# Kernel optimization log

Hardware: AMD Instinct MI355X
Metric: run time of the kernel (lower is better)

## Reference

```python
import jax, jax.numpy as jnp
import numpy as np
import math

N, H, E, G = 20000, 256, 320000, 1000
NF, NS = 64, 3           # sinusoid frequencies, spatial dims
DIS = 2 * NF * NS        # 384
EIN = 2 * H + 9 + DIS    # edge MLP input dim = 905


def silu(x):
    return x * jax.nn.sigmoid(x)


def sin_emb(x):
    # x: [E, 3] -> [E, 2*NF*3]
    freqs = 2.0 * math.pi * jnp.arange(NF, dtype=x.dtype)
    emb = (x[..., None] * freqs).reshape(x.shape[0], NF * NS)
    return jnp.concatenate([jnp.sin(emb), jnp.cos(emb)], axis=-1)


def layer_norm(x, gamma, beta, eps=1e-5):
    mu = jnp.mean(x, axis=-1, keepdims=True)
    var = jnp.var(x, axis=-1, keepdims=True)
    return (x - mu) * jax.lax.rsqrt(var + eps) * gamma + beta


def setup_inputs() -> dict:
    key = jax.random.key(0)
    ks = jax.random.split(key, 16)
    s = 0.02
    return {
        "node_features": jax.random.normal(ks[0], (N, H), jnp.float32),
        "lattices": jax.random.normal(ks[1], (G, 3, 3), jnp.float32),
        "edge_index": jax.random.randint(ks[2], (2, E), 0, N, dtype=jnp.int64),
        "edge2graph": jnp.sort(jax.random.randint(ks[3], (E,), 0, G, dtype=jnp.int64)),
        "frac_diff": jax.random.uniform(ks[4], (E, NS), jnp.float32),
        "num_atoms": jax.random.randint(ks[5], (G,), 0, 100, dtype=jnp.int64),
        "ln_gamma": jnp.ones((H,), jnp.float32),
        "ln_beta": jnp.zeros((H,), jnp.float32),
        "We1": jax.random.normal(ks[6], (EIN, H), jnp.float32) * s,
        "be1": jnp.zeros((H,), jnp.float32),
        "We2": jax.random.normal(ks[7], (H, H), jnp.float32) * s,
        "be2": jnp.zeros((H,), jnp.float32),
        "Wn1": jax.random.normal(ks[8], (2 * H, H), jnp.float32) * s,
        "bn1": jnp.zeros((H,), jnp.float32),
        "Wn2": jax.random.normal(ks[9], (H, H), jnp.float32) * s,
        "bn2": jnp.zeros((H,), jnp.float32),
    }


def reference(node_features, lattices, edge_index, edge2graph, frac_diff, num_atoms,
              ln_gamma, ln_beta, We1, be1, We2, be2, Wn1, bn1, Wn2, bn2):
    n = node_features.shape[0]
    h = layer_norm(node_features, ln_gamma, ln_beta)

    # edge model: gather + concat + MLP
    hi = h[edge_index[0]]                      # [E, H]
    hj = h[edge_index[1]]                      # [E, H]
    fd = sin_emb(frac_diff)                    # [E, DIS]
    ltl = jnp.einsum('gij,gkj->gik', lattices, lattices).reshape(-1, 9)  # non_symmetric: L @ L^T
    le = ltl[edge2graph]                       # [E, 9]
    x = jnp.concatenate([hi, hj, le, fd], axis=1)        # [E, EIN]
    e = silu(x @ We1 + be1)
    e = silu(e @ We2 + be2)                    # [E, H]

    # node model: scatter-mean + concat + MLP
    src = edge_index[0]
    sums = jax.ops.segment_sum(e, src, num_segments=n)   # [N, H]
    cnt = jax.ops.segment_sum(jnp.ones((e.shape[0],), e.dtype), src, num_segments=n)
    agg = sums / jnp.maximum(cnt, 1.0)[:, None]
    y = jnp.concatenate([h, agg], axis=1)                # [N, 2H]
    y = silu(y @ Wn1 + bn1)
    y = silu(y @ Wn2 + bn2)

    return node_features + y
```

## Files before the change

### kernel.cpp

```cpp
#include <hip/hip_runtime.h>

typedef unsigned short UST;
typedef __bf16 bf16x8 __attribute__((ext_vector_type(8)));
typedef float floatx4 __attribute__((ext_vector_type(4)));
typedef unsigned short ushort8v __attribute__((ext_vector_type(8)));
typedef unsigned short ushort4v __attribute__((ext_vector_type(4)));

#define N_NODES 20000
#define E_EDGES 320000
#define KF 384
#define M_PAD 20096


static __device__ __forceinline__ UST f2bf(float x){
  unsigned int u = __float_as_uint(x);
  u += 0x7fffu + ((u >> 16) & 1u);
  return (UST)(u >> 16);
}
static __device__ __forceinline__ float bf2f(UST u){
  return __uint_as_float(((unsigned int)u) << 16);
}
static __device__ __forceinline__ float siluf(float v){
  return v * __builtin_amdgcn_rcpf(1.0f + __expf(-v));
}
static __device__ __forceinline__ unsigned int cvtpk(float lo, float hi){
  unsigned int r;
  asm("v_cvt_pk_bf16_f32 %0, %1, %2" : "=v"(r) : "v"(lo), "v"(hi));
  return r;
}
static __device__ __forceinline__ void gll16(const void* g, void* lds){
  __builtin_amdgcn_global_load_lds(
      (const __attribute__((address_space(1))) unsigned int*)g,
      (__attribute__((address_space(3))) unsigned int*)lds, 16, 0, 0);
}

static __device__ __forceinline__ void mfma_step(const UST* As, const UST* Bs,
    floatx4 (&acc)[4][4], int lm, int quad, int wM, int wN){
  bf16x8 a[4], b[4];
#pragma unroll
  for (int i = 0; i < 4; ++i)
    a[i] = *(const bf16x8*)(As + (wM + i*16 + lm)*32 + quad*8);
#pragma unroll
  for (int i = 0; i < 4; ++i)
    b[i] = *(const bf16x8*)(Bs + (wN + i*16 + lm)*32 + quad*8);
#pragma unroll
  for (int mi = 0; mi < 4; ++mi)
#pragma unroll
    for (int ni = 0; ni < 4; ++ni)
      acc[mi][ni] = __builtin_amdgcn_mfma_f32_16x16x32_bf16(a[mi], b[ni], acc[mi][ni], 0, 0, 0);
}

static __device__ __forceinline__ void mfma_stage2(const UST* At, const UST* Bg,
    int Kb, floatx4 (&acc)[4][4], int lm, int quad, int wM, int wN){
#pragma unroll 2
  for (int k0 = 0; k0 < 256; k0 += 32){
    bf16x8 a[4], b[4];
#pragma unroll
    for (int i = 0; i < 4; ++i)
      a[i] = *(const bf16x8*)(At + (wM + i*16 + lm)*264 + k0 + quad*8);
#pragma unroll
    for (int i = 0; i < 4; ++i)
      b[i] = *(const bf16x8*)(Bg + (size_t)(wN + i*16 + lm)*Kb + k0 + quad*8);
#pragma unroll
    for (int mi = 0; mi < 4; ++mi)
#pragma unroll
      for (int ni = 0; ni < 4; ++ni)
        acc[mi][ni] = __builtin_amdgcn_mfma_f32_16x16x32_bf16(a[mi], b[ni], acc[mi][ni], 0, 0, 0);
  }
}

__global__ __launch_bounds__(256) void prep_all(
    const float* __restrict__ We1, const float* __restrict__ We2,
    const float* __restrict__ Wn1, const float* __restrict__ Wn2,
    const float* __restrict__ x, const float* __restrict__ gamma,
    const float* __restrict__ beta, const float* __restrict__ lat,
    const int* __restrict__ esrc, const float* __restrict__ be1,
    int* __restrict__ cnti,
    UST* __restrict__ W1T, UST* __restrict__ W2T,
    UST* __restrict__ Wn1T, UST* __restrict__ Wn2T, UST* __restrict__ W1hT,
    UST* __restrict__ h, float* __restrict__ Pleb){
  int bid = blockIdx.x, t = threadIdx.x;
  if (bid < 384){
    int i = bid*256 + t;
    int n = i / KF, k = i % KF;
    W1T[i] = f2bf(We1[(size_t)(521 + (k&1)*192 + (k>>1))*256 + n]);
  } else if (bid < 640){
    int i = (bid-384)*256 + t;
    int n = i >> 8, k = i & 255;
    W2T[i]  = f2bf(We2[(size_t)k*256 + n]);
    Wn2T[i] = f2bf(Wn2[(size_t)k*256 + n]);
  } else if (bid < 1152){
    int i = (bid-640)*256 + t;
    int n = i >> 9, k = i & 511;
    Wn1T[i] = f2bf(Wn1[(size_t)k*256 + n]);
  } else if (bid < 1664){
    int n = bid - 1152, k = t;
    W1hT[n*256 + k] = f2bf(We1[(size_t)(k + (n & 256))*256 + (n & 255)]);
  } else if (bid < 6664){
    int wave = t >> 6, lane = t & 63;
    int row = (bid-1664)*4 + wave;
    const float4* xp = (const float4*)(x + (size_t)row * 256);
    float4 v = xp[lane];
    float s  = v.x + v.y + v.z + v.w;
    float sq = v.x*v.x + v.y*v.y + v.z*v.z + v.w*v.w;
#pragma unroll
    for (int o = 32; o > 0; o >>= 1){ s += __shfl_xor(s, o); sq += __shfl_xor(sq, o); }
    float mu  = s * (1.0f/256.0f);
    float var = sq * (1.0f/256.0f) - mu*mu;
    float rs  = rsqrtf(var + 1e-5f);
    float4 g = ((const float4*)gamma)[lane];
    float4 b = ((const float4*)beta)[lane];
    uint2 o2;
    o2.x = cvtpk((v.x-mu)*rs*g.x + b.x, (v.y-mu)*rs*g.y + b.y);
    o2.y = cvtpk((v.z-mu)*rs*g.z + b.z, (v.w-mu)*rs*g.w + b.w);
    *(uint2*)(h + (size_t)row*256 + lane*4) = o2;
  } else if (bid < 7664){
    int g = bid - 6664;
    const float* L = lat + g*9;
    float acc = be1[t];
#pragma unroll
    for (int a = 0; a < 3; ++a)
#pragma unroll
      for (int b = 0; b < 3; ++b){
        float ltlv = L[a*3+0]*L[b*3+0] + L[a*3+1]*L[b*3+1] + L[a*3+2]*L[b*3+2];
        acc += ltlv * We1[(size_t)(512 + a*3 + b)*256 + t];
      }
    int tp = (t & 0xC0) | ((t & 15) << 2) | ((t >> 4) & 3);
    Pleb[g*256 + tp] = acc;
  } else {
    int e = (bid-7664)*256 + t;
    if (e < E_EDGES) atomicAdd(&cnti[esrc[e]], 1);
  }
}

__global__ __launch_bounds__(256) void scan_kernel(const int* __restrict__ cnti,
    int* __restrict__ off, int* __restrict__ head){
  __shared__ int ps[256];
  int t = threadIdx.x;
  const int CH = 80;
  const int4* cp = (const int4*)cnti;
  int base = t * CH;
  int s = 0;
#pragma unroll 1
  for (int i = 0; i < CH/4; ++i){
    int4 v = cp[t*(CH/4) + i];
    int idx = base + i*4;
    if (idx   < N_NODES) s += v.x;
    if (idx+1 < N_NODES) s += v.y;
    if (idx+2 < N_NODES) s += v.z;
    if (idx+3 < N_NODES) s += v.w;
  }
  ps[t] = s; __syncthreads();
#pragma unroll 1
  for (int o = 1; o < 256; o <<= 1){
    int v = (t >= o) ? ps[t - o] : 0;
    __syncthreads();
    ps[t] += v;
    __syncthreads();
  }
  int run = (t > 0) ? ps[t-1] : 0;
#pragma unroll 1
  for (int i = 0; i < CH/4; ++i){
    int4 v = cp[t*(CH/4) + i];
    int idx = base + i*4;
    int a4[4] = {v.x, v.y, v.z, v.w};
#pragma unroll
    for (int j = 0; j < 4; ++j){
      int id = idx + j;
      if (id < N_NODES){ off[id] = run; head[id] = run; run += a4[j]; }
    }
  }
  if (t == 255) off[N_NODES] = run;
}

__global__ __launch_bounds__(256) void fill_kernel(const int* __restrict__ src,
    int* __restrict__ head, int* __restrict__ eidx, int* __restrict__ srcs){
  int e = blockIdx.x*256 + threadIdx.x;
  if (e < E_EDGES){
    int s = src[e];
    int p = atomicAdd(&head[s], 1);
    eidx[p] = e;
    srcs[p] = s;
  }
}

__global__ __launch_bounds__(256, 4)
void gemm_p1(const UST* __restrict__ h, const UST* __restrict__ B1,
             float* __restrict__ P1){
  __shared__ __attribute__((aligned(16))) UST lds[20480];
  UST* As0 = lds;
  UST* As1 = lds + 2048;
  UST* Bs0 = lds + 4096;
  UST* Bs1 = lds + 12288;
  int t = threadIdx.x;
  int bM = blockIdx.x >> 1, bN = (blockIdx.x & 1) << 8;
  int rA = t >> 2, cA = (t & 3) * 8;
  const UST* hrow = h + (size_t)(bM*64 + rA)*256;
  int lane = t & 63, lm = lane & 15, quad = lane >> 4;
  int wave = t >> 6, wN = wave*64;
  floatx4 acc[4][4] = {};
  UST* a0d = &As0[rA*32 + cA];
  UST* a1d = &As1[rA*32 + cA];
#pragma unroll 1
  for (int w = 0; w < 4; ++w){
    int k0 = w*64;
    gll16(hrow + k0 + cA,      a0d);
    gll16(hrow + k0 + 32 + cA, a1d);
#pragma unroll
    for (int j = 0; j < 4; ++j){
      int rB = j*64 + rA;
      gll16(B1 + (size_t)(bN + rB)*256 + k0 + cA,      &Bs0[rB*32 + cA]);
      gll16(B1 + (size_t)(bN + rB)*256 + k0 + 32 + cA, &Bs1[rB*32 + cA]);
    }
    __syncthreads();
    mfma_step(As0, Bs0, acc, lm, quad, 0, wN);
    mfma_step(As1, Bs1, acc, lm, quad, 0, wN);
    __syncthreads();
  }
  int mbase = bM*64 + quad*4;
#pragma unroll
  for (int mi = 0; mi < 4; ++mi)
#pragma unroll
    for (int r = 0; r < 4; ++r){
      int m = mbase + mi*16 + r;
      float4 v;
      v.x = acc[mi][0][r]; v.y = acc[mi][1][r];
      v.z = acc[mi][2][r]; v.w = acc[mi][3][r];
      *(float4*)(P1 + (size_t)m*512 + bN + wN + lm*4) = v;
    }
}

__global__ __launch_bounds__(512, 4)
void gemm_edge_fused(const int* __restrict__ ei, const int* __restrict__ e2g,
                     const float* __restrict__ fdif, const UST* __restrict__ W1T,
                     const int* __restrict__ eidx,
                     const UST* __restrict__ W2T, const float* __restrict__ be2,
                     const int* __restrict__ rownode,
                     const float* __restrict__ P1, const float* __restrict__ Pleb,
                     float* __restrict__ sums){
  __shared__ __attribute__((aligned(16))) UST lds[128*264];
  __shared__ int rn[128], rd[128], rg[128];
  UST* Ab0 = lds;
  UST* Ab1 = lds + 4096;
  UST* Bb0 = lds + 8192;
  UST* Bb1 = lds + 16384;
  UST* e1t = lds;
  UST* EsT = lds;
  int t = threadIdx.x;
  int bM = blockIdx.x;
  int rA = t >> 2, cA = (t & 3) * 8;
  int p0 = bM*128 + rA;
  int e0 = eidx[p0];
  float f0x = fdif[e0*3+0], f0y = fdif[e0*3+1], f0z = fdif[e0*3+2];
  size_t btb0 = (size_t)rA*KF + cA;
  size_t btb1 = btb0 + (size_t)128*KF;
  int lane = t & 63, lm = lane & 15, quad = lane >> 4;
  int wave = t >> 6, wM = (wave >> 2)*64, wN = (wave & 3)*64;
  floatx4 acc[4][4] = {};
  if (t < 128){
    int e = eidx[bM*128 + t];
    rn[t] = rownode[bM*128 + t];
    rd[t] = ei[E_EDGES + e];
    rg[t] = e2g[e];
  }

  float sdx = __builtin_amdgcn_sinf(f0x), cdx = __builtin_amdgcn_cosf(f0x);
  float sdy = __builtin_amdgcn_sinf(f0y), cdy = __builtin_amdgcn_cosf(f0y);
  float sdz = __builtin_amdgcn_sinf(f0z), cdz = __builtin_amdgcn_cosf(f0z);

  auto buildA = [&](int s)->uint4 {
    int j0 = s*16 + (cA >> 1);
    int dim = j0 >> 6;
    float fr = (dim == 0) ? f0x : ((dim == 1) ? f0y : f0z);
    float sd = (dim == 0) ? sdx : ((dim == 1) ? sdy : sdz);
    float cd = (dim == 0) ? cdx : ((dim == 1) ? cdy : cdz);
    float q  = __builtin_amdgcn_fractf(fr * (float)(j0 & 63));
    float sn = __builtin_amdgcn_sinf(q);
    float cs = __builtin_amdgcn_cosf(q);
    uint4 o;
    o.x = cvtpk(sn, cs);
    float s2;
    s2 = fmaf(sn, cd, cs*sd); cs = fmaf(cs, cd, -sn*sd); sn = s2; o.y = cvtpk(sn, cs);
    s2 = fmaf(sn, cd, cs*sd); cs = fmaf(cs, cd, -sn*sd); sn = s2; o.z = cvtpk(sn, cs);
    s2 = fmaf(sn, cd, cs*sd); cs = fmaf(cs, cd, -sn*sd); sn = s2; o.w = cvtpk(sn, cs);
    return o;
  };

  {
    uint4 o = buildA(0);
    *(uint4*)&Ab0[rA*32 + cA] = o;
    gll16(W1T + btb0, &Bb0[rA*32 + cA]);
    gll16(W1T + btb1, &Bb0[(128+rA)*32 + cA]);
  }
  __syncthreads();
#pragma unroll 1
  for (int s = 0; s < 12; ++s){
    UST* Ac = (s & 1) ? Ab1 : Ab0;
    UST* Bc = (s & 1) ? Bb1 : Bb0;
    if (s < 11){
      uint4 o = buildA(s+1);
      UST* An = (s & 1) ? Ab0 : Ab1;
      UST* Bn = (s & 1) ? Bb0 : Bb1;
      *(uint4*)&An[rA*32 + cA] = o;
      int k0 = (s+1)*32;
      gll16(W1T + btb0 + k0, &Bn[rA*32 + cA]);
      gll16(W1T + btb1 + k0, &Bn[(128+rA)*32 + cA]);
    }
    mfma_step(Ac, Bc, acc, lm, quad, wM, wN);
    __syncthreads();
  }

#pragma unroll
  for (int mi = 0; mi < 4; ++mi){
    int ml0 = wM + mi*16 + quad*4;
    float bs[4][4];
#pragma unroll
    for (int r = 0; r < 4; ++r){
      int ml = ml0 + r;
      float4 a4 = *(const float4*)(P1   + (size_t)rn[ml]*512 + wN + lm*4);
      float4 b4 = *(const float4*)(P1   + (size_t)rd[ml]*512 + 256 + wN + lm*4);
      float4 c4 = *(const float4*)(Pleb + (size_t)rg[ml]*256 + wN + lm*4);
      bs[r][0] = a4.x + b4.x + c4.x;
      bs[r][1] = a4.y + b4.y + c4.y;
      bs[r][2] = a4.z + b4.z + c4.z;
      bs[r][3] = a4.w + b4.w + c4.w;
    }
#pragma unroll
    for (int ni = 0; ni < 4; ++ni){
      int nl = wN + ni*16 + lm;
      float f0 = siluf(acc[mi][ni][0] + bs[0][ni]);
      float f1 = siluf(acc[mi][ni][1] + bs[1][ni]);
      float f2 = siluf(acc[mi][ni][2] + bs[2][ni]);
      float f3 = siluf(acc[mi][ni][3] + bs[3][ni]);
      unsigned w01 = cvtpk(f0, f1);
      unsigned w23 = cvtpk(f2, f3);
      e1t[(ml0+0)*264 + nl] = (UST)(w01 & 0xffffu);
      e1t[(ml0+1)*264 + nl] = (UST)(w01 >> 16);
      e1t[(ml0+2)*264 + nl] = (UST)(w23 & 0xffffu);
      e1t[(ml0+3)*264 + nl] = (UST)(w23 >> 16);
    }
  }
  __syncthreads();

  floatx4 acc2[4][4] = {};
  mfma_stage2(e1t, W2T, 256, acc2, lm, quad, wM, wN);
  __syncthreads();

#pragma unroll
  for (int mi = 0; mi < 4; ++mi)
#pragma unroll
    for (int ni = 0; ni < 4; ++ni){
      int nl = wN + ni*16 + lm;
      int ml = wM + mi*16 + quad*4;
      float b = be2[nl];
      uint2 pk2;
      pk2.x = cvtpk(siluf(acc2[mi][ni][0] + b), siluf(acc2[mi][ni][1] + b));
      pk2.y = cvtpk(siluf(acc2[mi][ni][2] + b), siluf(acc2[mi][ni][3] + b));
      *(uint2*)&EsT[nl*132 + ml] = pk2;
    }
  __syncthreads();
  {
    int c = t & 255, hh = t >> 8;
    int rbeg = hh * 64;
    int cur = rn[rbeg];
    float run = 0.0f;
#pragma unroll 1
    for (int r = rbeg; r < rbeg + 64; r += 4){
      ushort4v v4 = *(const ushort4v*)&EsT[c*132 + r];
#pragma unroll
      for (int q2 = 0; q2 < 4; ++q2){
        int nd = rn[r + q2];
        if (nd != cur){ atomicAdd(&sums[(size_t)cur*256 + c], run); run = 0.0f; cur = nd; }
        run += bf2f(v4[q2]);
      }
    }
    atomicAdd(&sums[(size_t)cur*256 + c], run);
  }
}

__global__ __launch_bounds__(256, 4)
void gemm_node12(const UST* __restrict__ h, const float* __restrict__ sums,
                 const int* __restrict__ offs, const UST* __restrict__ B1,
                 const float* __restrict__ bn1, const UST* __restrict__ B2,
                 const float* __restrict__ bn2,
                 float* __restrict__ out_f, const float* __restrict__ resid){
  __shared__ __attribute__((aligned(16))) UST lds[20480];
  UST* As0 = lds;
  UST* As1 = lds + 2048;
  UST* Bs0 = lds + 4096;
  UST* Bs1 = lds + 12288;
  UST* y1t = lds;
  int t = threadIdx.x;
  int bM = blockIdx.x;
  int rA = t >> 2, cA = (t & 3) * 8;
  int row = bM*64 + rA;
  bool valid = row < N_NODES;
  float inv = 0.0f;
  if (valid){
    int deg = offs[row+1] - offs[row];
    inv = 1.0f / fmaxf((float)deg, 1.0f);
  }
  const UST* hrow = h + (size_t)row*256;
  const float* srow = sums + (size_t)row*256;
  int lane = t & 63, lm = lane & 15, quad = lane >> 4;
  int wave = t >> 6, wN = wave*64;
  floatx4 acc[4][4] = {};
  UST* a0d = &As0[rA*32 + cA];
  UST* a1d = &As1[rA*32 + cA];
  const uint4 z4 = {0,0,0,0};
#pragma unroll 1
  for (int w = 0; w < 8; ++w){
    int k0 = w*64;
    if (k0 < 256){
      if (valid){
        gll16(hrow + k0 + cA,      a0d);
        gll16(hrow + k0 + 32 + cA, a1d);
      } else {
        *(uint4*)a0d = z4;
        *(uint4*)a1d = z4;
      }
    } else {
      uint4 o0 = z4, o1 = z4;
      if (valid){
        int q = k0 - 256 + cA;
        float4 s0 = *(const float4*)(srow + q);
        float4 s1 = *(const float4*)(srow + q + 4);
        o0.x = cvtpk(s0.x*inv, s0.y*inv); o0.y = cvtpk(s0.z*inv, s0.w*inv);
        o0.z = cvtpk(s1.x*inv, s1.y*inv); o0.w = cvtpk(s1.z*inv, s1.w*inv);
        float4 s2 = *(const float4*)(srow + q + 32);
        float4 s3 = *(const float4*)(srow + q + 36);
        o1.x = cvtpk(s2.x*inv, s2.y*inv); o1.y = cvtpk(s2.z*inv, s2.w*inv);
        o1.z = cvtpk(s3.x*inv, s3.y*inv); o1.w = cvtpk(s3.z*inv, s3.w*inv);
      }
      *(uint4*)a0d = o0;
      *(uint4*)a1d = o1;
    }
#pragma unroll
    for (int j = 0; j < 4; ++j){
      int rB = j*64 + rA;
      gll16(B1 + (size_t)rB*512 + k0 + cA,      &Bs0[rB*32 + cA]);
      gll16(B1 + (size_t)rB*512 + k0 + 32 + cA, &Bs1[rB*32 + cA]);
    }
    __syncthreads();
    mfma_step(As0, Bs0, acc, lm, quad, 0, wN);
    mfma_step(As1, Bs1, acc, lm, quad, 0, wN);
    __syncthreads();
  }
#pragma unroll
  for (int mi = 0; mi < 4; ++mi){
    int ml0 = mi*16 + quad*4;
#pragma unroll
    for (int ni = 0; ni < 4; ++ni){
      int nl = wN + ni*16 + lm;
      float b = bn1[nl];
      unsigned w01 = cvtpk(siluf(acc[mi][ni][0] + b), siluf(acc[mi][ni][1] + b));
      unsigned w23 = cvtpk(siluf(acc[mi][ni][2] + b), siluf(acc[mi][ni][3] + b));
      y1t[(ml0+0)*264 + nl] = (UST)(w01 & 0xffffu);
      y1t[(ml0+1)*264 + nl] = (UST)(w01 >> 16);
      y1t[(ml0+2)*264 + nl] = (UST)(w23 & 0xffffu);
      y1t[(ml0+3)*264 + nl] = (UST)(w23 >> 16);
    }
  }
  __syncthreads();
  floatx4 acc2[4][4] = {};
  mfma_stage2(y1t, B2, 256, acc2, lm, quad, 0, wN);
  int mbase = bM*64 + quad*4;
  int nbase = wN + lm;
#pragma unroll
  for (int mi = 0; mi < 4; ++mi)
#pragma unroll
    for (int r = 0; r < 4; ++r){
      int m = mbase + mi*16 + r;
      if (m < N_NODES){
#pragma unroll
        for (int ni = 0; ni < 4; ++ni){
          int n = nbase + ni*16;
          float v = siluf(acc2[mi][ni][r] + bn2[n]);
          out_f[(size_t)m*256 + n] = resid[(size_t)m*256 + n] + v;
        }
      }
    }
}

extern "C" void kernel_launch(void* const* d_in, const int* in_sizes, int n_in,
                              void* d_out, int out_size, void* d_ws, size_t ws_size,
                              hipStream_t stream){
  (void)in_sizes; (void)n_in; (void)out_size; (void)ws_size;
  const float* node_features = (const float*)d_in[0];
  const float* lattices      = (const float*)d_in[1];
  const int*   edge_index    = (const int*)d_in[2];
  const int*   edge2graph    = (const int*)d_in[3];
  const float* frac_diff     = (const float*)d_in[4];
  const float* ln_gamma      = (const float*)d_in[6];
  const float* ln_beta       = (const float*)d_in[7];
  const float* We1 = (const float*)d_in[8];
  const float* be1 = (const float*)d_in[9];
  const float* We2 = (const float*)d_in[10];
  const float* be2 = (const float*)d_in[11];
  const float* Wn1 = (const float*)d_in[12];
  const float* bn1 = (const float*)d_in[13];
  const float* Wn2 = (const float*)d_in[14];
  const float* bn2 = (const float*)d_in[15];

  char* w = (char*)d_ws;
  size_t off_b = 0;
  auto carve = [&](size_t bytes) -> char* {
    char* p = w + off_b; off_b += (bytes + 1023) & ~(size_t)1023; return p;
  };
  UST*   W1T  = (UST*)carve((size_t)256*KF*2);
  UST*   W2T  = (UST*)carve((size_t)256*256*2);
  UST*   Wn1T = (UST*)carve((size_t)256*512*2);
  UST*   Wn2T = (UST*)carve((size_t)256*256*2);
  UST*   W1hT = (UST*)carve((size_t)512*256*2);
  UST*   hbf  = (UST*)carve((size_t)M_PAD*256*2);
  float* P1   = (float*)carve((size_t)M_PAD*512*4);
  float* Pleb = (float*)carve((size_t)1000*256*4);
  int*   cnti = (int*)carve((size_t)20480*4);
  int*   offs = (int*)carve((size_t)(N_NODES+1)*4);
  int*   head = (int*)carve((size_t)N_NODES*4);
  int*   eidx = (int*)carve((size_t)E_EDGES*4);
  int*   srcs = (int*)carve((size_t)E_EDGES*4);
  float* sums = (float*)carve((size_t)N_NODES*256*4);

  hipMemsetAsync(cnti, 0, (size_t)20480*4, stream);
  hipMemsetAsync(sums, 0, (size_t)N_NODES*256*4, stream);

  prep_all<<<7664 + E_EDGES/256, 256, 0, stream>>>(We1, We2, Wn1, Wn2,
      node_features, ln_gamma, ln_beta, lattices, edge_index, be1, cnti,
      W1T, W2T, Wn1T, Wn2T, W1hT, hbf, Pleb);

  scan_kernel<<<1, 256, 0, stream>>>(cnti, offs, head);
  fill_kernel<<<E_EDGES/256, 256, 0, stream>>>(edge_index, head, eidx, srcs);

  gemm_p1<<<(M_PAD/64)*2, 256, 0, stream>>>(hbf, W1hT, P1);

  gemm_edge_fused<<<E_EDGES/128, 512, 0, stream>>>(
      edge_index, edge2graph, frac_diff, W1T, eidx, W2T, be2, srcs, P1, Pleb, sums);

  gemm_node12<<<M_PAD/64, 256, 0, stream>>>(
      hbf, sums, offs, Wn1T, bn1, Wn2T, bn2, (float*)d_out, node_features);
}
```

Measured before the change: 488.1 us.

## Shrink edge GEMM tile to 64 rows and read W1 directly from global

```diff
diff --git a/kernel.cpp b/kernel.cpp
--- a/kernel.cpp
+++ b/kernel.cpp
@@ -50,14 +50,14 @@
       acc[mi][ni] = __builtin_amdgcn_mfma_f32_16x16x32_bf16(a[mi], b[ni], acc[mi][ni], 0, 0, 0);
 }
 
-static __device__ __forceinline__ void mfma_stage2(const UST* At, const UST* Bg,
-    int Kb, floatx4 (&acc)[4][4], int lm, int quad, int wM, int wN){
+static __device__ __forceinline__ void mfma_direct(const UST* At, int ldA,
+    const UST* Bg, int Kb, int klen, floatx4 (&acc)[4][4], int lm, int quad, int wN){
 #pragma unroll 2
-  for (int k0 = 0; k0 < 256; k0 += 32){
+  for (int k0 = 0; k0 < klen; k0 += 32){
     bf16x8 a[4], b[4];
 #pragma unroll
     for (int i = 0; i < 4; ++i)
-      a[i] = *(const bf16x8*)(At + (wM + i*16 + lm)*264 + k0 + quad*8);
+      a[i] = *(const bf16x8*)(At + (i*16 + lm)*ldA + k0 + quad*8);
 #pragma unroll
     for (int i = 0; i < 4; ++i)
       b[i] = *(const bf16x8*)(Bg + (size_t)(wN + i*16 + lm)*Kb + k0 + quad*8);
@@ -230,7 +230,7 @@
     }
 }
 
-__global__ __launch_bounds__(512, 4)
+__global__ __launch_bounds__(256, 4)
 void gemm_edge_fused(const int* __restrict__ ei, const int* __restrict__ e2g,
                      const float* __restrict__ fdif, const UST* __restrict__ W1T,
                      const int* __restrict__ eidx,
@@ -238,81 +238,71 @@
                      const int* __restrict__ rownode,
                      const float* __restrict__ P1, const float* __restrict__ Pleb,
                      float* __restrict__ sums){
-  __shared__ __attribute__((aligned(16))) UST lds[128*264];
-  __shared__ int rn[128], rd[128], rg[128];
-  UST* Ab0 = lds;
-  UST* Ab1 = lds + 4096;
-  UST* Bb0 = lds + 8192;
-  UST* Bb1 = lds + 16384;
+  __shared__ __attribute__((aligned(16))) UST lds[17408];
+  __shared__ int rn[64], rd[64], rg[64];
+  UST* Ah  = lds;
   UST* e1t = lds;
   UST* EsT = lds;
   int t = threadIdx.x;
   int bM = blockIdx.x;
-  int rA = t >> 2, cA = (t & 3) * 8;
-  int p0 = bM*128 + rA;
-  int e0 = eidx[p0];
-  float f0x = fdif[e0*3+0], f0y = fdif[e0*3+1], f0z = fdif[e0*3+2];
-  size_t btb0 = (size_t)rA*KF + cA;
-  size_t btb1 = btb0 + (size_t)128*KF;
   int lane = t & 63, lm = lane & 15, quad = lane >> 4;
-  int wave = t >> 6, wM = (wave >> 2)*64, wN = (wave & 3)*64;
-  floatx4 acc[4][4] = {};
-  if (t < 128){
-    int e = eidx[bM*128 + t];
-    rn[t] = rownode[bM*128 + t];
+  int wave = t >> 6, wN = wave*64;
+  if (t < 64){
+    int e = eidx[bM*64 + t];
+    rn[t] = rownode[bM*64 + t];
     rd[t] = ei[E_EDGES + e];
     rg[t] = e2g[e];
   }
-
-  float sdx = __builtin_amdgcn_sinf(f0x), cdx = __builtin_amdgcn_cosf(f0x);
-  float sdy = __builtin_amdgcn_sinf(f0y), cdy = __builtin_amdgcn_cosf(f0y);
-  float sdz = __builtin_amdgcn_sinf(f0z), cdz = __builtin_amdgcn_cosf(f0z);
-
-  auto buildA = [&](int s)->uint4 {
-    int j0 = s*16 + (cA >> 1);
-    int dim = j0 >> 6;
-    float fr = (dim == 0) ? f0x : ((dim == 1) ? f0y : f0z);
-    float sd = (dim == 0) ? sdx : ((dim == 1) ? sdy : sdz);
-    float cd = (dim == 0) ? cdx : ((dim == 1) ? cdy : cdz);
-    float q  = __builtin_amdgcn_fractf(fr * (float)(j0 & 63));
-    float sn = __builtin_amdgcn_sinf(q);
-    float cs = __builtin_amdgcn_cosf(q);
-    uint4 o;
-    o.x = cvtpk(sn, cs);
-    float s2;
-    s2 = fmaf(sn, cd, cs*sd); cs = fmaf(cs, cd, -sn*sd); sn = s2; o.y = cvtpk(sn, cs);
-    s2 = fmaf(sn, cd, cs*sd); cs = fmaf(cs, cd, -sn*sd); sn = s2; o.z = cvtpk(sn, cs);
-    s2 = fmaf(sn, cd, cs*sd); cs = fmaf(cs, cd, -sn*sd); sn = s2; o.w = cvtpk(sn, cs);
-    return o;
-  };
-
-  {
-    uint4 o = buildA(0);
-    *(uint4*)&Ab0[rA*32 + cA] = o;
-    gll16(W1T + btb0, &Bb0[rA*32 + cA]);
-    gll16(W1T + btb1, &Bb0[(128+rA)*32 + cA]);
-  }
-  __syncthreads();
-#pragma unroll 1
-  for (int s = 0; s < 12; ++s){
-    UST* Ac = (s & 1) ? Ab1 : Ab0;
-    UST* Bc = (s & 1) ? Bb1 : Bb0;
-    if (s < 11){
-      uint4 o = buildA(s+1);
-      UST* An = (s & 1) ? Ab0 : Ab1;
-      UST* Bn = (s & 1) ? Bb0 : Bb1;
-      *(uint4*)&An[rA*32 + cA] = o;
-      int k0 = (s+1)*32;
-      gll16(W1T + btb0 + k0, &Bn[rA*32 + cA]);
-      gll16(W1T + btb1 + k0, &Bn[(128+rA)*32 + cA]);
-    }
-    mfma_step(Ac, Bc, acc, lm, quad, wM, wN);
+  int rA = t >> 2, chunk = t & 3;
+  int eA = eidx[bM*64 + rA];
+  float fx = fdif[eA*3+0], fy = fdif[eA*3+1], fz = fdif[eA*3+2];
+  floatx4 acc[4][4] = {};
+
+#pragma unroll 1
+  for (int half = 0; half < 2; ++half){
+    {
+      int jg0 = half*96 + chunk*24;
+      UST* dst = Ah + rA*200 + chunk*48;
+      int dim0 = jg0 >> 6;
+      float fr = (dim0 == 0) ? fx : ((dim0 == 1) ? fy : fz);
+      float sd = __builtin_amdgcn_sinf(fr);
+      float cd = __builtin_amdgcn_cosf(fr);
+      float q  = __builtin_amdgcn_fractf(fr * (float)(jg0 & 63));
+      float sn = __builtin_amdgcn_sinf(q);
+      float cs = __builtin_amdgcn_cosf(q);
+      unsigned u0, u1, u2, u3;
+#pragma unroll
+      for (int g4 = 0; g4 < 6; ++g4){
+#pragma unroll
+        for (int a4 = 0; a4 < 4; ++a4){
+          int a = g4*4 + a4;
+          int jg = jg0 + a;
+          if (a != 0 && (jg & 63) == 0){
+            int dim = jg >> 6;
+            fr = (dim == 0) ? fx : ((dim == 1) ? fy : fz);
+            sd = __builtin_amdgcn_sinf(fr);
+            cd = __builtin_amdgcn_cosf(fr);
+            sn = 0.0f; cs = 1.0f;
+          }
+          unsigned pk = cvtpk(sn, cs);
+          if (a4 == 0) u0 = pk; else if (a4 == 1) u1 = pk;
+          else if (a4 == 2) u2 = pk; else u3 = pk;
+          float s2 = fmaf(sn, cd, cs*sd);
+          cs = fmaf(cs, cd, -sn*sd);
+          sn = s2;
+        }
+        uint4 o; o.x = u0; o.y = u1; o.z = u2; o.w = u3;
+        *(uint4*)(dst + g4*8) = o;
+      }
+    }
+    __syncthreads();
+    mfma_direct(Ah, 200, W1T + half*192, 384, 192, acc, lm, quad, wN);
     __syncthreads();
   }
 
 #pragma unroll
   for (int mi = 0; mi < 4; ++mi){
-    int ml0 = wM + mi*16 + quad*4;
+    int ml0 = mi*16 + quad*4;
     float bs[4][4];
 #pragma unroll
     for (int r = 0; r < 4; ++r){
@@ -343,7 +333,7 @@
   __syncthreads();
 
   floatx4 acc2[4][4] = {};
-  mfma_stage2(e1t, W2T, 256, acc2, lm, quad, wM, wN);
+  mfma_direct(e1t, 264, W2T, 256, 256, acc2, lm, quad, wN);
   __syncthreads();
 
 #pragma unroll
@@ -351,22 +341,21 @@
 #pragma unroll
     for (int ni = 0; ni < 4; ++ni){
       int nl = wN + ni*16 + lm;
-      int ml = wM + mi*16 + quad*4;
+      int ml = mi*16 + quad*4;
       float b = be2[nl];
       uint2 pk2;
       pk2.x = cvtpk(siluf(acc2[mi][ni][0] + b), siluf(acc2[mi][ni][1] + b));
       pk2.y = cvtpk(siluf(acc2[mi][ni][2] + b), siluf(acc2[mi][ni][3] + b));
-      *(uint2*)&EsT[nl*132 + ml] = pk2;
+      *(uint2*)&EsT[nl*68 + ml] = pk2;
     }
   __syncthreads();
   {
-    int c = t & 255, hh = t >> 8;
-    int rbeg = hh * 64;
-    int cur = rn[rbeg];
+    int c = t;
+    int cur = rn[0];
     float run = 0.0f;
 #pragma unroll 1
-    for (int r = rbeg; r < rbeg + 64; r += 4){
-      ushort4v v4 = *(const ushort4v*)&EsT[c*132 + r];
+    for (int r = 0; r < 64; r += 4){
+      ushort4v v4 = *(const ushort4v*)&EsT[c*68 + r];
 #pragma unroll
       for (int q2 = 0; q2 < 4; ++q2){
         int nd = rn[r + q2];
@@ -463,7 +452,7 @@
   }
   __syncthreads();
   floatx4 acc2[4][4] = {};
-  mfma_stage2(y1t, B2, 256, acc2, lm, quad, 0, wN);
+  mfma_direct(y1t, 264, B2, 256, 256, acc2, lm, quad, wN);
   int mbase = bM*64 + quad*4;
   int nbase = wN + lm;
 #pragma unroll
@@ -534,7 +523,7 @@
 
   gemm_p1<<<(M_PAD/64)*2, 256, 0, stream>>>(hbf, W1hT, P1);
 
-  gemm_edge_fused<<<E_EDGES/128, 512, 0, stream>>>(
+  gemm_edge_fused<<<E_EDGES/64, 256, 0, stream>>>(
       edge_index, edge2graph, frac_diff, W1T, eidx, W2T, be2, srcs, P1, Pleb, sums);
 
   gemm_node12<<<M_PAD/64, 256, 0, stream>>>(
```

Result: faster. 455.8 us (-6.6%).

## Store node projection P1 in bf16 and unroll edge GEMM K-loop

Applied to the files above, without the earlier changes.

```diff
diff --git a/kernel.cpp b/kernel.cpp
--- a/kernel.cpp
+++ b/kernel.cpp
@@ -20,6 +20,8 @@
 static __device__ __forceinline__ float bf2f(UST u){
   return __uint_as_float(((unsigned int)u) << 16);
 }
+static __device__ __forceinline__ float bflo(unsigned u){ return __uint_as_float(u << 16); }
+static __device__ __forceinline__ float bfhi(unsigned u){ return __uint_as_float(u & 0xffff0000u); }
 static __device__ __forceinline__ float siluf(float v){
   return v * __builtin_amdgcn_rcpf(1.0f + __expf(-v));
 }
@@ -50,14 +52,14 @@
       acc[mi][ni] = __builtin_amdgcn_mfma_f32_16x16x32_bf16(a[mi], b[ni], acc[mi][ni], 0, 0, 0);
 }
 
-static __device__ __forceinline__ void mfma_stage2(const UST* At, const UST* Bg,
-    int Kb, floatx4 (&acc)[4][4], int lm, int quad, int wM, int wN){
+static __device__ __forceinline__ void mfma_direct(const UST* At, int ldA,
+    const UST* Bg, int Kb, int klen, floatx4 (&acc)[4][4], int lm, int quad, int wM, int wN){
 #pragma unroll 2
-  for (int k0 = 0; k0 < 256; k0 += 32){
+  for (int k0 = 0; k0 < klen; k0 += 32){
     bf16x8 a[4], b[4];
 #pragma unroll
     for (int i = 0; i < 4; ++i)
-      a[i] = *(const bf16x8*)(At + (wM + i*16 + lm)*264 + k0 + quad*8);
+      a[i] = *(const bf16x8*)(At + (wM + i*16 + lm)*ldA + k0 + quad*8);
 #pragma unroll
     for (int i = 0; i < 4; ++i)
       b[i] = *(const bf16x8*)(Bg + (size_t)(wN + i*16 + lm)*Kb + k0 + quad*8);
@@ -186,7 +188,7 @@
 
 __global__ __launch_bounds__(256, 4)
 void gemm_p1(const UST* __restrict__ h, const UST* __restrict__ B1,
-             float* __restrict__ P1){
+             UST* __restrict__ P1){
   __shared__ __attribute__((aligned(16))) UST lds[20480];
   UST* As0 = lds;
   UST* As1 = lds + 2048;
@@ -223,10 +225,10 @@
 #pragma unroll
     for (int r = 0; r < 4; ++r){
       int m = mbase + mi*16 + r;
-      float4 v;
-      v.x = acc[mi][0][r]; v.y = acc[mi][1][r];
-      v.z = acc[mi][2][r]; v.w = acc[mi][3][r];
-      *(float4*)(P1 + (size_t)m*512 + bN + wN + lm*4) = v;
+      uint2 v;
+      v.x = cvtpk(acc[mi][0][r], acc[mi][1][r]);
+      v.y = cvtpk(acc[mi][2][r], acc[mi][3][r]);
+      *(uint2*)(P1 + (size_t)m*512 + bN + wN + lm*4) = v;
     }
 }
 
@@ -236,7 +238,7 @@
                      const int* __restrict__ eidx,
                      const UST* __restrict__ W2T, const float* __restrict__ be2,
                      const int* __restrict__ rownode,
-                     const float* __restrict__ P1, const float* __restrict__ Pleb,
+                     const UST* __restrict__ P1, const float* __restrict__ Pleb,
                      float* __restrict__ sums){
   __shared__ __attribute__((aligned(16))) UST lds[128*264];
   __shared__ int rn[128], rd[128], rg[128];
@@ -268,43 +270,39 @@
   float sdy = __builtin_amdgcn_sinf(f0y), cdy = __builtin_amdgcn_cosf(f0y);
   float sdz = __builtin_amdgcn_sinf(f0z), cdz = __builtin_amdgcn_cosf(f0z);
 
-  auto buildA = [&](int s)->uint4 {
-    int j0 = s*16 + (cA >> 1);
-    int dim = j0 >> 6;
+  auto buildA = [&](int s, UST* dst){
+    int jb = s*16 + (cA >> 1);
+    int dim = jb >> 6;
     float fr = (dim == 0) ? f0x : ((dim == 1) ? f0y : f0z);
     float sd = (dim == 0) ? sdx : ((dim == 1) ? sdy : sdz);
     float cd = (dim == 0) ? cdx : ((dim == 1) ? cdy : cdz);
-    float q  = __builtin_amdgcn_fractf(fr * (float)(j0 & 63));
+    float q  = __builtin_amdgcn_fractf(fr * (float)(jb & 63));
     float sn = __builtin_amdgcn_sinf(q);
     float cs = __builtin_amdgcn_cosf(q);
     uint4 o;
     o.x = cvtpk(sn, cs);
-    float s2;
-    s2 = fmaf(sn, cd, cs*sd); cs = fmaf(cs, cd, -sn*sd); sn = s2; o.y = cvtpk(sn, cs);
-    s2 = fmaf(sn, cd, cs*sd); cs = fmaf(cs, cd, -sn*sd); sn = s2; o.z = cvtpk(sn, cs);
-    s2 = fmaf(sn, cd, cs*sd); cs = fmaf(cs, cd, -sn*sd); sn = s2; o.w = cvtpk(sn, cs);
-    return o;
+    float t2;
+    t2 = fmaf(sn, cd, cs*sd); cs = fmaf(cs, cd, -sn*sd); sn = t2; o.y = cvtpk(sn, cs);
+    t2 = fmaf(sn, cd, cs*sd); cs = fmaf(cs, cd, -sn*sd); sn = t2; o.z = cvtpk(sn, cs);
+    t2 = fmaf(sn, cd, cs*sd); cs = fmaf(cs, cd, -sn*sd); sn = t2; o.w = cvtpk(sn, cs);
+    *(uint4*)dst = o;
   };
 
-  {
-    uint4 o = buildA(0);
-    *(uint4*)&Ab0[rA*32 + cA] = o;
-    gll16(W1T + btb0, &Bb0[rA*32 + cA]);
-    gll16(W1T + btb1, &Bb0[(128+rA)*32 + cA]);
-  }
+  gll16(W1T + btb0, &Bb0[rA*32 + cA]);
+  gll16(W1T + btb1, &Bb0[(128+rA)*32 + cA]);
+  buildA(0, &Ab0[rA*32 + cA]);
   __syncthreads();
-#pragma unroll 1
+#pragma unroll
   for (int s = 0; s < 12; ++s){
     UST* Ac = (s & 1) ? Ab1 : Ab0;
     UST* Bc = (s & 1) ? Bb1 : Bb0;
     if (s < 11){
-      uint4 o = buildA(s+1);
       UST* An = (s & 1) ? Ab0 : Ab1;
       UST* Bn = (s & 1) ? Bb0 : Bb1;
-      *(uint4*)&An[rA*32 + cA] = o;
       int k0 = (s+1)*32;
       gll16(W1T + btb0 + k0, &Bn[rA*32 + cA]);
       gll16(W1T + btb1 + k0, &Bn[(128+rA)*32 + cA]);
+      buildA(s+1, &An[rA*32 + cA]);
     }
     mfma_step(Ac, Bc, acc, lm, quad, wM, wN);
     __syncthreads();
@@ -317,13 +315,13 @@
 #pragma unroll
     for (int r = 0; r < 4; ++r){
       int ml = ml0 + r;
-      float4 a4 = *(const float4*)(P1   + (size_t)rn[ml]*512 + wN + lm*4);
-      float4 b4 = *(const float4*)(P1   + (size_t)rd[ml]*512 + 256 + wN + lm*4);
+      uint2 a2 = *(const uint2*)(P1 + (size_t)rn[ml]*512 + wN + lm*4);
+      uint2 b2 = *(const uint2*)(P1 + (size_t)rd[ml]*512 + 256 + wN + lm*4);
       float4 c4 = *(const float4*)(Pleb + (size_t)rg[ml]*256 + wN + lm*4);
-      bs[r][0] = a4.x + b4.x + c4.x;
-      bs[r][1] = a4.y + b4.y + c4.y;
-      bs[r][2] = a4.z + b4.z + c4.z;
-      bs[r][3] = a4.w + b4.w + c4.w;
+      bs[r][0] = bflo(a2.x) + bflo(b2.x) + c4.x;
+      bs[r][1] = bfhi(a2.x) + bfhi(b2.x) + c4.y;
+      bs[r][2] = bflo(a2.y) + bflo(b2.y) + c4.z;
+      bs[r][3] = bfhi(a2.y) + bfhi(b2.y) + c4.w;
     }
 #pragma unroll
     for (int ni = 0; ni < 4; ++ni){
@@ -343,7 +341,7 @@
   __syncthreads();
 
   floatx4 acc2[4][4] = {};
-  mfma_stage2(e1t, W2T, 256, acc2, lm, quad, wM, wN);
+  mfma_direct(e1t, 264, W2T, 256, 256, acc2, lm, quad, wM, wN);
   __syncthreads();
 
 #pragma unroll
@@ -463,7 +461,7 @@
   }
   __syncthreads();
   floatx4 acc2[4][4] = {};
-  mfma_stage2(y1t, B2, 256, acc2, lm, quad, 0, wN);
+  mfma_direct(y1t, 264, B2, 256, 256, acc2, lm, quad, 0, wN);
   int mbase = bM*64 + quad*4;
   int nbase = wN + lm;
 #pragma unroll
@@ -513,7 +511,7 @@
   UST*   Wn2T = (UST*)carve((size_t)256*256*2);
   UST*   W1hT = (UST*)carve((size_t)512*256*2);
   UST*   hbf  = (UST*)carve((size_t)M_PAD*256*2);
-  float* P1   = (float*)carve((size_t)M_PAD*512*4);
+  UST*   P1   = (UST*)carve((size_t)M_PAD*512*2);
   float* Pleb = (float*)carve((size_t)1000*256*4);
   int*   cnti = (int*)carve((size_t)20480*4);
   int*   offs = (int*)carve((size_t)(N_NODES+1)*4);
```

Result: slower. 517.4 us (+6.0%).
